# Performance work log

Measured on AMD Instinct MI355X. Metric: run time of the kernel, lower is better.

Reference implementation:

```python
import jax, jax.numpy as jnp
import numpy as np

NUM_NODES = 17
NUM_REL = 8  # 4 edge types, doubled with reverse edges
IN_DIM = HID_DIM = OUT_DIM = 2048


def _build_graph():
    # Hardcoded brain graph from _build_brain_graph()
    # signals 0-5, emotions 6-11, cognitions 12-16
    src = np.array([0,0,1,1,2,2,3,3,4,4,5,5,          # signal->emotion (type 0)
                    6,6,7,7,8,8,8,9,9,10,11,11,       # emotion->cognition (type 1)
                    6,9,7,10,8,11,6,8,7,8,            # emotion<->emotion (type 2)
                    0,1,2])                            # signal->cognition (type 3)
    dst = np.array([7,10,6,9,9,7,10,7,6,9,9,6,
                    15,12,14,13,12,13,16,16,12,14,16,12,
                    9,6,10,7,11,8,8,6,8,7,
                    12,12,13])
    typ = np.array([0]*12 + [1]*12 + [2]*10 + [3]*3)
    # edge_index = cat([E, E.flip(0)]); edge_type = cat([t, t + 4])
    ei = np.stack([np.concatenate([src, dst]), np.concatenate([dst, src])])
    et = np.concatenate([typ, typ + 4])
    return jnp.asarray(ei, jnp.int32), jnp.asarray(et, jnp.int32)


def setup_inputs() -> dict:
    key = jax.random.key(0)
    ks = jax.random.split(key, 6)
    s = 0.02  # init scale
    edge_index, edge_type = _build_graph()
    return {
        'node_emb': jax.random.normal(ks[0], (NUM_NODES, IN_DIM), jnp.float32),
        'signal_features': jax.random.normal(ks[1], (6, IN_DIM), jnp.float32),
        'W1': jax.random.normal(ks[2], (NUM_REL, IN_DIM, HID_DIM), jnp.float32) * s,
        'root1': jax.random.normal(ks[3], (IN_DIM, HID_DIM), jnp.float32) * s,
        'bias1': jnp.zeros((HID_DIM,), jnp.float32),
        'W2': jax.random.normal(ks[4], (NUM_REL, HID_DIM, OUT_DIM), jnp.float32) * s,
        'root2': jax.random.normal(ks[5], (HID_DIM, OUT_DIM), jnp.float32) * s,
        'bias2': jnp.zeros((OUT_DIM,), jnp.float32),
        'edge_index': edge_index,
        'edge_type': edge_type,
    }


def _rgcn(x, W, root, bias, src, dst, etype):
    """PyG-style RGCNConv: per-relation linear + per-relation mean aggregation + root + bias."""
    # Transform all 17 nodes by all relations at once: [R, N, H] (tiny activation, avoids
    # gathering a [E, d, h] weight tensor per edge).
    xW = jnp.einsum('nd,rdh->rnh', x, W)
    msg = xW[etype, src]                                  # [E, H]
    seg = etype * NUM_NODES + dst                         # segment per (relation, target)
    sums = jax.ops.segment_sum(msg, seg, num_segments=NUM_REL * NUM_NODES)
    cnt = jax.ops.segment_sum(jnp.ones((msg.shape[0],), x.dtype), seg,
                              num_segments=NUM_REL * NUM_NODES)
    mean = sums / jnp.maximum(cnt, 1.0)[:, None]          # per-relation mean aggr
    agg = mean.reshape(NUM_REL, NUM_NODES, -1).sum(0)     # sum over relations
    return agg + x @ root + bias


def reference(node_emb, signal_features, W1, root1, bias1, W2, root2, bias2,
              edge_index, edge_type):
    src, dst = edge_index[0], edge_index[1]
    # h = node_emb(arange(17)); h[:6] = signal_features
    h = node_emb.at[:signal_features.shape[0]].set(signal_features)
    h1 = jax.nn.relu(_rgcn(h, W1, root1, bias1, src, dst, edge_type))
    # dropout is identity in eval mode
    h2 = _rgcn(h1, W2, root2, bias2, src, dst, edge_type)
    return h2
```

## Files before the change

### kernel.cpp

```cpp
#include <hip/hip_runtime.h>
#include <hip/hip_bf16.h>

#define D 2048
#define NTASK 55
#define NAGG 38
#define CHUNK 64
#define NCH 32

__constant__ int c_grp[10] = {0, 4, 9, 15, 17, 23, 29, 35, 38, 55};

__constant__ int c_src[74] = {
    1,4,5,  0,2,3,  1,2,4,5,  0,3,
    6,8,9,11,  7,8,  7,10,  6,  8,9,11,
    9,8,  10,8,  11,6,7,  6,  7,  8,
    0,1,  2,
    7,10,  6,9,  9,7,  10,7,  6,9,  9,6,
    15,12,  14,13,  12,13,16,  16,12,  14,  16,12,
    9,8,  10,8,  11,6,7,  6,  7,  8,
    12, 12, 13
};
__constant__ int c_off[39] = {
    0,3,6,10,12, 16,18,20,21,24, 26,28,31,32,33, 34,36,
    37,39,41,43,45,47, 49,51,53,56,58,59, 61,63,65,68,69,70, 71,72,73,74
};

__constant__ int c_node_tasks[38] = {
    17,35,  18,36,  19,37,  20,  21,  22,
    0,9,23,29,  1,10,24,30,  11,25,31,  2,12,26,32,  3,13,27,33,  14,28,34,
    4,15,  5,16,  6,  7,  8
};
__constant__ int c_node_off[18] = {0,2,4,6,7,8,9,13,17,20,24,28,31,33,35,36,37,38};

__global__ __launch_bounds__(256) void prep_kernel(
        const float* __restrict__ emb, const float* __restrict__ sig,
        float* __restrict__ U) {
    int t = blockIdx.x;
    int tid = threadIdx.x;
    if (t >= NAGG) {
        int v = t - NAGG;
        const float* h = (v < 6) ? sig + (size_t)v * D : emb + (size_t)v * D;
        for (int c = tid; c < D; c += 256)
            U[(size_t)t * D + c] = h[c];
    } else {
        int o0 = c_off[t], o1 = c_off[t + 1];
        float inv = 1.f / (float)(o1 - o0);
        for (int c = tid; c < D; c += 256) {
            float s = 0.f;
            for (int o = o0; o < o1; ++o) {
                int sn = c_src[o];
                const float* h = (sn < 6) ? sig + (size_t)sn * D : emb + (size_t)sn * D;
                s += h[c];
            }
            U[(size_t)t * D + c] = s * inv;
        }
    }
}

#define LOADB(buf, base_row)                                                    \
    _Pragma("unroll") for (int i_ = 0; i_ < 8; ++i_)                            \
        buf[i_] = *reinterpret_cast<const float4*>(Wbase + (size_t)((base_row) + i_) * D);

#define FMAB(buf, base_row)                                                     \
    _Pragma("unroll") for (int i_ = 0; i_ < 8; ++i_) {                          \
        _Pragma("unroll") for (int t_ = 0; t_ < NG; ++t_) {                     \
            float u_ = su[t_ * CHUNK + (base_row) + i_];                        \
            acc[t_].x = fmaf(u_, buf[i_].x, acc[t_].x);                         \
            acc[t_].y = fmaf(u_, buf[i_].y, acc[t_].y);                         \
            acc[t_].z = fmaf(u_, buf[i_].z, acc[t_].z);                         \
            acc[t_].w = fmaf(u_, buf[i_].w, acc[t_].w);                         \
        }                                                                       \
    }

template <int NG>
__device__ __forceinline__ void gemm_inner(
        const float* __restrict__ Wbase, const float* su,
        float* __restrict__ Pout) {
    float4 acc[NG];
#pragma unroll
    for (int t = 0; t < NG; ++t) acc[t] = make_float4(0.f, 0.f, 0.f, 0.f);
    float4 wa[8], wb[8];
    LOADB(wa, 0)
    LOADB(wb, 8)
    FMAB(wa, 0)   LOADB(wa, 16)
    FMAB(wb, 8)   LOADB(wb, 24)
    FMAB(wa, 16)  LOADB(wa, 32)
    FMAB(wb, 24)  LOADB(wb, 40)
    FMAB(wa, 32)  LOADB(wa, 48)
    FMAB(wb, 40)  LOADB(wb, 56)
    FMAB(wa, 48)
    FMAB(wb, 56)
#pragma unroll
    for (int t = 0; t < NG; ++t)
        *reinterpret_cast<float4*>(Pout + (size_t)t * D) = acc[t];
}

__global__ __launch_bounds__(256) void gemm_kernel(
        const float* __restrict__ U, const float* __restrict__ W,
        const float* __restrict__ root, float* __restrict__ P) {
    int b = blockIdx.x;
    int g = b >> 6;
    int r = b & 63;
    int ct = r & 1;
    int ch = r >> 1;
    int d0 = ch * CHUNK;
    int col = ct * 1024 + threadIdx.x * 4;
    const float* Wg = (g < 8) ? W + (size_t)g * D * D : root;
    int tb = c_grp[g];
    int ng = c_grp[g + 1] - tb;

    __shared__ float su[17 * CHUNK];
    for (int i = threadIdx.x; i < ng * CHUNK; i += 256) {
        int t = i >> 6, dd = i & (CHUNK - 1);
        su[i] = U[(size_t)(tb + t) * D + d0 + dd];
    }
    __syncthreads();

    const float* Wbase = Wg + (size_t)d0 * D + col;
    float* Pout = P + ((size_t)ch * NTASK + tb) * D + col;

    switch (ng) {
        case 2:  gemm_inner<2>(Wbase, su, Pout); break;
        case 3:  gemm_inner<3>(Wbase, su, Pout); break;
        case 4:  gemm_inner<4>(Wbase, su, Pout); break;
        case 5:  gemm_inner<5>(Wbase, su, Pout); break;
        case 6:  gemm_inner<6>(Wbase, su, Pout); break;
        default: gemm_inner<17>(Wbase, su, Pout); break;
    }
}

__global__ __launch_bounds__(256) void mid1_kernel(
        const float* __restrict__ P, const float* __restrict__ bias,
        float* __restrict__ h1) {
    int idx = blockIdx.x * 256 + threadIdx.x;
    int v = idx >> 11, col = idx & (D - 1);
    float s = bias[col];
    for (int o = c_node_off[v]; o < c_node_off[v + 1]; ++o) {
        const float* p = P + (size_t)c_node_tasks[o] * D + col;
#pragma unroll
        for (int ch = 0; ch < NCH; ++ch) s += p[(size_t)ch * NTASK * D];
    }
    {
        const float* p = P + (size_t)(NAGG + v) * D + col;
#pragma unroll
        for (int ch = 0; ch < NCH; ++ch) s += p[(size_t)ch * NTASK * D];
    }
    h1[idx] = fmaxf(s, 0.f);
}

__global__ __launch_bounds__(256) void u2_kernel(
        const float* __restrict__ h1, float* __restrict__ U) {
    int idx = blockIdx.x * 256 + threadIdx.x;
    int t = idx >> 11, col = idx & (D - 1);
    if (t >= NAGG) {
        U[idx] = h1[(size_t)(t - NAGG) * D + col];
    } else {
        int o0 = c_off[t], o1 = c_off[t + 1];
        float s = 0.f;
        for (int o = o0; o < o1; ++o)
            s += h1[(size_t)c_src[o] * D + col];
        U[idx] = s / (float)(o1 - o0);
    }
}

__global__ __launch_bounds__(256) void fin_kernel(
        const float* __restrict__ P, const float* __restrict__ bias,
        float* __restrict__ out) {
    int idx = blockIdx.x * 256 + threadIdx.x;
    int v = idx >> 11, col = idx & (D - 1);
    float s = bias[col];
    for (int o = c_node_off[v]; o < c_node_off[v + 1]; ++o) {
        const float* p = P + (size_t)c_node_tasks[o] * D + col;
#pragma unroll
        for (int ch = 0; ch < NCH; ++ch) s += p[(size_t)ch * NTASK * D];
    }
    {
        const float* p = P + (size_t)(NAGG + v) * D + col;
#pragma unroll
        for (int ch = 0; ch < NCH; ++ch) s += p[(size_t)ch * NTASK * D];
    }
    out[idx] = s;
}

extern "C" void kernel_launch(void* const* d_in, const int* in_sizes, int n_in,
                              void* d_out, int out_size, void* d_ws, size_t ws_size,
                              hipStream_t stream) {
    const float* emb   = (const float*)d_in[0];
    const float* sig   = (const float*)d_in[1];
    const float* W1    = (const float*)d_in[2];
    const float* root1 = (const float*)d_in[3];
    const float* b1    = (const float*)d_in[4];
    const float* W2    = (const float*)d_in[5];
    const float* root2 = (const float*)d_in[6];
    const float* b2    = (const float*)d_in[7];
    float* out = (float*)d_out;

    float* U  = (float*)d_ws;
    float* h1 = U + (size_t)NTASK * D;
    float* P  = h1 + (size_t)17 * D;

    prep_kernel<<<NTASK, 256, 0, stream>>>(emb, sig, U);
    gemm_kernel<<<9 * 2 * NCH, 256, 0, stream>>>(U, W1, root1, P);
    mid1_kernel<<<17 * D / 256, 256, 0, stream>>>(P, b1, h1);
    u2_kernel<<<NTASK * D / 256, 256, 0, stream>>>(h1, U);
    gemm_kernel<<<9 * 2 * NCH, 256, 0, stream>>>(U, W2, root2, P);
    fin_kernel<<<17 * D / 256, 256, 0, stream>>>(P, b2, out);
}
```

Before: 362.7 us.

## Fuse neighbor-mean prep into GEMM kernel and double K-chunk size

The separate prep and u2 kernels that built the per-relation mean inputs are removed. Each GEMM block now loads the 17 node rows for its K-chunk into shared memory and computes the mean aggregates there. CHUNK is doubled to 128 and NCH halved to 16, which halves the number of GEMM blocks (288 instead of 576) and the split-K partials that the reduction kernels read. It also vectorises the shared-memory reads of the inputs. The trade-offs are two fewer launches and less partial-sum traffic against lower GEMM parallelism, redundant gathering in every block, and more shared memory per block.

Measured after the change: 385.9 us. 6.4% more time.

```diff
diff --git a/kernel.cpp b/kernel.cpp
--- a/kernel.cpp
+++ b/kernel.cpp
@@ -4,12 +4,12 @@
 #define D 2048
 #define NTASK 55
 #define NAGG 38
-#define CHUNK 64
-#define NCH 32
+#define CHUNK 128
+#define NCH 16
 
 __constant__ int c_grp[10] = {0, 4, 9, 15, 17, 23, 29, 35, 38, 55};
 
-__constant__ int c_src[74] = {
+__constant__ int c_src[91] = {
     1,4,5,  0,2,3,  1,2,4,5,  0,3,
     6,8,9,11,  7,8,  7,10,  6,  8,9,11,
     9,8,  10,8,  11,6,7,  6,  7,  8,
@@ -17,11 +17,13 @@
     7,10,  6,9,  9,7,  10,7,  6,9,  9,6,
     15,12,  14,13,  12,13,16,  16,12,  14,  16,12,
     9,8,  10,8,  11,6,7,  6,  7,  8,
-    12, 12, 13
+    12, 12, 13,
+    0,1,2,3,4,5,6,7,8,9,10,11,12,13,14,15,16
 };
-__constant__ int c_off[39] = {
+__constant__ int c_off[56] = {
     0,3,6,10,12, 16,18,20,21,24, 26,28,31,32,33, 34,36,
-    37,39,41,43,45,47, 49,51,53,56,58,59, 61,63,65,68,69,70, 71,72,73,74
+    37,39,41,43,45,47, 49,51,53,56,58,59, 61,63,65,68,69,70, 71,72,73,74,
+    75,76,77,78,79,80,81,82,83,84,85,86,87,88,89,90,91
 };
 
 __constant__ int c_node_tasks[38] = {
@@ -31,75 +33,52 @@
 };
 __constant__ int c_node_off[18] = {0,2,4,6,7,8,9,13,17,20,24,28,31,33,35,36,37,38};
 
-__global__ __launch_bounds__(256) void prep_kernel(
-        const float* __restrict__ emb, const float* __restrict__ sig,
-        float* __restrict__ U) {
-    int t = blockIdx.x;
-    int tid = threadIdx.x;
-    if (t >= NAGG) {
-        int v = t - NAGG;
-        const float* h = (v < 6) ? sig + (size_t)v * D : emb + (size_t)v * D;
-        for (int c = tid; c < D; c += 256)
-            U[(size_t)t * D + c] = h[c];
-    } else {
-        int o0 = c_off[t], o1 = c_off[t + 1];
-        float inv = 1.f / (float)(o1 - o0);
-        for (int c = tid; c < D; c += 256) {
-            float s = 0.f;
-            for (int o = o0; o < o1; ++o) {
-                int sn = c_src[o];
-                const float* h = (sn < 6) ? sig + (size_t)sn * D : emb + (size_t)sn * D;
-                s += h[c];
-            }
-            U[(size_t)t * D + c] = s * inv;
-        }
-    }
-}
 
-#define LOADB(buf, base_row)                                                    \
+#define LD8(buf, base)                                                          \
     _Pragma("unroll") for (int i_ = 0; i_ < 8; ++i_)                            \
-        buf[i_] = *reinterpret_cast<const float4*>(Wbase + (size_t)((base_row) + i_) * D);
+        buf[i_] = *reinterpret_cast<const float4*>(Wb + (size_t)((base) + i_) * D);
 
-#define FMAB(buf, base_row)                                                     \
-    _Pragma("unroll") for (int i_ = 0; i_ < 8; ++i_) {                          \
-        _Pragma("unroll") for (int t_ = 0; t_ < NG; ++t_) {                     \
-            float u_ = su[t_ * CHUNK + (base_row) + i_];                        \
-            acc[t_].x = fmaf(u_, buf[i_].x, acc[t_].x);                         \
-            acc[t_].y = fmaf(u_, buf[i_].y, acc[t_].y);                         \
-            acc[t_].z = fmaf(u_, buf[i_].z, acc[t_].z);                         \
-            acc[t_].w = fmaf(u_, buf[i_].w, acc[t_].w);                         \
+#define FMA8(buf, base)                                                         \
+    _Pragma("unroll") for (int t_ = 0; t_ < NG; ++t_) {                         \
+        float4 u0 = *reinterpret_cast<const float4*>(&su[t_ * CHUNK + (base)]); \
+        float4 u1 = *reinterpret_cast<const float4*>(&su[t_ * CHUNK + (base) + 4]); \
+        float uu[8] = {u0.x,u0.y,u0.z,u0.w,u1.x,u1.y,u1.z,u1.w};                \
+        _Pragma("unroll") for (int i_ = 0; i_ < 8; ++i_) {                      \
+            acc[t_].x = fmaf(uu[i_], buf[i_].x, acc[t_].x);                     \
+            acc[t_].y = fmaf(uu[i_], buf[i_].y, acc[t_].y);                     \
+            acc[t_].z = fmaf(uu[i_], buf[i_].z, acc[t_].z);                     \
+            acc[t_].w = fmaf(uu[i_], buf[i_].w, acc[t_].w);                     \
         }                                                                       \
     }
 
 template <int NG>
 __device__ __forceinline__ void gemm_inner(
-        const float* __restrict__ Wbase, const float* su,
-        float* __restrict__ Pout) {
+        const float* __restrict__ Wb, const float* su, float* __restrict__ Pout) {
     float4 acc[NG];
 #pragma unroll
     for (int t = 0; t < NG; ++t) acc[t] = make_float4(0.f, 0.f, 0.f, 0.f);
     float4 wa[8], wb[8];
-    LOADB(wa, 0)
-    LOADB(wb, 8)
-    FMAB(wa, 0)   LOADB(wa, 16)
-    FMAB(wb, 8)   LOADB(wb, 24)
-    FMAB(wa, 16)  LOADB(wa, 32)
-    FMAB(wb, 24)  LOADB(wb, 40)
-    FMAB(wa, 32)  LOADB(wa, 48)
-    FMAB(wb, 40)  LOADB(wb, 56)
-    FMAB(wa, 48)
-    FMAB(wb, 56)
+    LD8(wa, 0)
+    LD8(wb, 8)
+#pragma unroll
+    for (int b = 0; b < CHUNK; b += 16) {
+        FMA8(wa, b)
+        if (b + 16 < CHUNK) LD8(wa, b + 16)
+        FMA8(wb, b + 8)
+        if (b + 24 < CHUNK) LD8(wb, b + 24)
+    }
 #pragma unroll
     for (int t = 0; t < NG; ++t)
         *reinterpret_cast<float4*>(Pout + (size_t)t * D) = acc[t];
 }
 
 __global__ __launch_bounds__(256) void gemm_kernel(
-        const float* __restrict__ U, const float* __restrict__ W,
-        const float* __restrict__ root, float* __restrict__ P) {
+        const float* __restrict__ hA, const float* __restrict__ hB,
+        const float* __restrict__ W, const float* __restrict__ root,
+        float* __restrict__ P) {
     int b = blockIdx.x;
-    int g = b >> 6;
-    int r = b & 63;
+    int g = b >> 5;
+    int r = b & 31;
     int ct = r & 1;
     int ch = r >> 1;
     int d0 = ch * CHUNK;
@@ -108,27 +87,38 @@
     int tb = c_grp[g];
     int ng = c_grp[g + 1] - tb;
 
-    __shared__ float su[17 * CHUNK];
+    __shared__ __align__(16) float hh[17 * CHUNK];
+    __shared__ __align__(16) float su[17 * CHUNK];
+
+    for (int i = threadIdx.x; i < 17 * CHUNK; i += 256) {
+        int v = i >> 7, dd = i & (CHUNK - 1);
+        const float* h = (v < 6) ? hB : hA;
+        hh[i] = h[(size_t)v * D + d0 + dd];
+    }
+    __syncthreads();
     for (int i = threadIdx.x; i < ng * CHUNK; i += 256) {
-        int t = i >> 6, dd = i & (CHUNK - 1);
-        su[i] = U[(size_t)(tb + t) * D + d0 + dd];
+        int t = i >> 7, dd = i & (CHUNK - 1);
+        int o0 = c_off[tb + t], o1 = c_off[tb + t + 1];
+        float s = 0.f;
+        for (int o = o0; o < o1; ++o) s += hh[c_src[o] * CHUNK + dd];
+        su[i] = s / (float)(o1 - o0);
     }
     __syncthreads();
 
-    const float* Wbase = Wg + (size_t)d0 * D + col;
+    const float* Wb = Wg + (size_t)d0 * D + col;
     float* Pout = P + ((size_t)ch * NTASK + tb) * D + col;
 
     switch (ng) {
-        case 2:  gemm_inner<2>(Wbase, su, Pout); break;
-        case 3:  gemm_inner<3>(Wbase, su, Pout); break;
-        case 4:  gemm_inner<4>(Wbase, su, Pout); break;
-        case 5:  gemm_inner<5>(Wbase, su, Pout); break;
-        case 6:  gemm_inner<6>(Wbase, su, Pout); break;
-        default: gemm_inner<17>(Wbase, su, Pout); break;
+        case 2:  gemm_inner<2>(Wb, su, Pout); break;
+        case 3:  gemm_inner<3>(Wb, su, Pout); break;
+        case 4:  gemm_inner<4>(Wb, su, Pout); break;
+        case 5:  gemm_inner<5>(Wb, su, Pout); break;
+        case 6:  gemm_inner<6>(Wb, su, Pout); break;
+        default: gemm_inner<17>(Wb, su, Pout); break;
     }
 }
 
-__global__ __launch_bounds__(256) void mid1_kernel(
+__global__ __launch_bounds__(256) void mid_kernel(
         const float* __restrict__ P, const float* __restrict__ bias,
         float* __restrict__ h1) {
     int idx = blockIdx.x * 256 + threadIdx.x;
@@ -145,21 +135,6 @@
         for (int ch = 0; ch < NCH; ++ch) s += p[(size_t)ch * NTASK * D];
     }
     h1[idx] = fmaxf(s, 0.f);
-}
-
-__global__ __launch_bounds__(256) void u2_kernel(
-        const float* __restrict__ h1, float* __restrict__ U) {
-    int idx = blockIdx.x * 256 + threadIdx.x;
-    int t = idx >> 11, col = idx & (D - 1);
-    if (t >= NAGG) {
-        U[idx] = h1[(size_t)(t - NAGG) * D + col];
-    } else {
-        int o0 = c_off[t], o1 = c_off[t + 1];
-        float s = 0.f;
-        for (int o = o0; o < o1; ++o)
-            s += h1[(size_t)c_src[o] * D + col];
-        U[idx] = s / (float)(o1 - o0);
-    }
 }
 
 __global__ __launch_bounds__(256) void fin_kernel(
@@ -194,14 +169,11 @@
     const float* b2    = (const float*)d_in[7];
     float* out = (float*)d_out;
 
-    float* U  = (float*)d_ws;
-    float* h1 = U + (size_t)NTASK * D;
+    float* h1 = (float*)d_ws;
     float* P  = h1 + (size_t)17 * D;
 
-    prep_kernel<<<NTASK, 256, 0, stream>>>(emb, sig, U);
-    gemm_kernel<<<9 * 2 * NCH, 256, 0, stream>>>(U, W1, root1, P);
-    mid1_kernel<<<17 * D / 256, 256, 0, stream>>>(P, b1, h1);
-    u2_kernel<<<NTASK * D / 256, 256, 0, stream>>>(h1, U);
-    gemm_kernel<<<9 * 2 * NCH, 256, 0, stream>>>(U, W2, root2, P);
+    gemm_kernel<<<9 * 2 * NCH, 256, 0, stream>>>(emb, sig, W1, root1, P);
+    mid_kernel<<<17 * D / 256, 256, 0, stream>>>(P, b1, h1);
+    gemm_kernel<<<9 * 2 * NCH, 256, 0, stream>>>(h1, h1, W2, root2, P);
     fin_kernel<<<17 * D / 256, 256, 0, stream>>>(P, b2, out);
 }
```
